# Optimization experiments

Hardware: AMD Instinct MI355X
Metric: run time of the kernel (lower is better)

## Reference

```python
import jax, jax.numpy as jnp
import numpy as np

N_USERS = 60000
N_ITEMS = 40000
N_NODES = N_USERS + N_ITEMS
N_EDGES = 1_000_000
D = 64
BN_EPS = 1e-3  # tf.layers.batch_normalization default epsilon


def setup_inputs() -> dict:
    key = jax.random.key(0)
    ks = jax.random.split(key, 16)
    s = 1.0 / np.sqrt(D)  # uniform-ish init scale for [D,D] weights
    w = lambda k: (jax.random.uniform(k, (D, D), jnp.float32, -1.0, 1.0) * s)
    return {
        "u_features": jax.random.normal(ks[0], (N_USERS, D), jnp.float32),
        "v_features": jax.random.normal(ks[1], (N_ITEMS, D), jnp.float32),
        "edge_start": jax.random.randint(ks[2], (N_EDGES,), 0, N_NODES, jnp.int32),
        "edge_end": jax.random.randint(ks[3], (N_EDGES,), 0, N_NODES, jnp.int32),
        "Ui1": w(ks[4]), "Uj1": w(ks[5]), "Vi1": w(ks[6]), "Vj1": w(ks[7]),
        "bu1": jnp.zeros((D,), jnp.float32), "bv1": jnp.zeros((D,), jnp.float32),
        "Ui2": w(ks[8]), "Uj2": w(ks[9]), "Vi2": w(ks[10]), "Vj2": w(ks[11]),
        "bu2": jnp.zeros((D,), jnp.float32), "bv2": jnp.zeros((D,), jnp.float32),
        "R": w(ks[12]),
        "gamma1": jnp.ones((D,), jnp.float32), "beta1": jnp.zeros((D,), jnp.float32),
        "gamma2": jnp.ones((D,), jnp.float32), "beta2": jnp.zeros((D,), jnp.float32),
    }


def _stage(x, Ui, Uj, Vi, Vj, bu, bv, e_start, e_end, n_nodes):
    # gate = sigmoid(E_end@(x Vi) + E_start@(x Vj) + bv)   -> edge gather
    gate = jax.nn.sigmoid((x @ Vi)[e_end] + (x @ Vj)[e_start] + bv)  # [E, D]
    msg = gate * (x @ Ui)[e_start]                                    # [E, D]
    # x Uj + E_end.T @ msg + bu   -> scatter-add to destination nodes
    agg = jax.ops.segment_sum(msg, e_end, num_segments=n_nodes)       # [N, D]
    return x @ Uj + agg + bu


def _batchnorm(x, gamma, beta):
    mean = jnp.mean(x, axis=0)
    var = jnp.var(x, axis=0)
    return gamma * (x - mean) * jax.lax.rsqrt(var + BN_EPS) + beta


def reference(u_features, v_features, edge_start, edge_end,
              Ui1, Uj1, Vi1, Vj1, bu1, bv1,
              Ui2, Uj2, Vi2, Vj2, bu2, bv2,
              R, gamma1, beta1, gamma2, beta2):
    num_users = u_features.shape[0]
    x_in = jnp.concatenate([u_features, v_features], axis=0)  # [N, D]
    n = x_in.shape[0]
    x = _stage(x_in, Ui1, Uj1, Vi1, Vj1, bu1, bv1, edge_start, edge_end, n)
    x = jax.nn.relu(_batchnorm(x, gamma1, beta1))
    x = _stage(x, Ui2, Uj2, Vi2, Vj2, bu2, bv2, edge_start, edge_end, n)
    x = _batchnorm(x, gamma2, beta2)
    x = jax.nn.relu(x + x_in @ R)  # residual branch
    return x[:num_users], x[num_users:]
```

## Files before the change

### kernel.cpp

```cpp
#include <hip/hip_runtime.h>
#include <hip/hip_bf16.h>

#define NUSERS 60000
#define NNODES 100000
#define DD 64
#define NGB 1563
#define GMM 782
#define NBUK 196
#define ESB 2048

typedef __hip_bfloat16 bf16;
using bf16x8 = __attribute__((ext_vector_type(8))) short;
using f32x4  = __attribute__((ext_vector_type(4))) float;

__device__ __forceinline__ float b2f(bf16 x) { return __bfloat162float(x); }
__device__ __forceinline__ bf16 f2b(float x) { return __float2bfloat16(x); }
__device__ __forceinline__ unsigned short fbits(float x) {
    union { bf16 b; unsigned short u; } cv; cv.b = f2b(x); return cv.u;
}
__device__ __forceinline__ float us2f(unsigned short h) {
    union { unsigned u; float f; } t; t.u = (unsigned)h << 16; return t.f;
}
__device__ __forceinline__ float lo_bf16(unsigned w) {
    union { unsigned u; float f; } t; t.u = w << 16; return t.f;
}
__device__ __forceinline__ float hi_bf16(unsigned w) {
    union { unsigned u; float f; } t; t.u = w & 0xFFFF0000u; return t.f;
}
__device__ __forceinline__ float ldf(const void* p, size_t i, int isbf) {
    if (isbf) return b2f(((const bf16*)p)[i]);
    return ((const float*)p)[i];
}
__device__ __forceinline__ unsigned pack2(float a, float b) {
    return (unsigned)fbits(a) | ((unsigned)fbits(b) << 16);
}
__device__ __forceinline__ unsigned pr2(float x0, float x1, float a0, float a1,
                                        float b0, float b1) {
    float t0 = a0 * x0 + b0, t1 = a1 * x1 + b1;
    t0 = t0 > 0.f ? t0 : 0.f;
    t1 = t1 > 0.f ? t1 : 0.f;
    return pack2(t0, t1);
}

__global__ void k_sniff(const unsigned short* __restrict__ h,
                        int* __restrict__ flag, float* __restrict__ red,
                        int* __restrict__ btot)
{
    __shared__ int cs[256];
    int t = threadIdx.x;
    int cnt = 0;
    for (int i = t; i < 1024; i += 256) {
        int e = (h[2 * i] >> 7) & 0xFF;
        cnt += (e >= 100 && e <= 140) ? 1 : 0;
    }
    cs[t] = cnt;
    __syncthreads();
    for (int s = 128; s > 0; s >>= 1) {
        if (t < s) cs[t] += cs[t + s];
        __syncthreads();
    }
    if (t == 0) flag[0] = (cs[0] > 512) ? 1 : 0;
    red[t] = 0.f;
    btot[t] = 0;
}

__global__ __launch_bounds__(256) void k_bhist(const int* __restrict__ ee,
                                               int* __restrict__ btot, int E)
{
    __shared__ int h[256];
    int t = threadIdx.x;
    h[t] = 0;
    __syncthreads();
    for (int e = blockIdx.x * 256 + t; e < E; e += gridDim.x * 256)
        atomicAdd(&h[ee[e] >> 9], 1);
    __syncthreads();
    if (h[t]) atomicAdd(&btot[t], h[t]);
}

__global__ void k_bscan(const int* __restrict__ btot, int* __restrict__ bbase,
                        int* __restrict__ bcursor)
{
    __shared__ int sd[256];
    int t = threadIdx.x;
    int v = btot[t];
    sd[t] = v;
    __syncthreads();
    for (int off = 1; off < 256; off <<= 1) {
        int x = (t >= off) ? sd[t - off] : 0;
        __syncthreads();
        sd[t] += x;
        __syncthreads();
    }
    int excl = sd[t] - v;
    bbase[t] = excl;
    bcursor[t] = excl;
}

__global__ __launch_bounds__(256) void k_bscatter(
    const int* __restrict__ es, const int* __restrict__ ee,
    int* __restrict__ bcursor, unsigned* __restrict__ ebuf, int E)
{
    __shared__ int h[256], gb[256], lr[256];
    int t = threadIdx.x;
    h[t] = 0;
    lr[t] = 0;
    __syncthreads();
    int base = blockIdx.x * ESB;
    unsigned ent[8];
    int bk[8];
#pragma unroll
    for (int i = 0; i < 8; i++) {
        int e = base + t + i * 256;
        if (e < E) {
            int s = es[e], d = ee[e];
            bk[i] = d >> 9;
            ent[i] = (unsigned)s | ((unsigned)(d & 511) << 20);
            atomicAdd(&h[bk[i]], 1);
        } else bk[i] = -1;
    }
    __syncthreads();
    if (h[t]) gb[t] = atomicAdd(&bcursor[t], h[t]);
    __syncthreads();
#pragma unroll
    for (int i = 0; i < 8; i++) {
        if (bk[i] >= 0) {
            int r = atomicAdd(&lr[bk[i]], 1);
            ebuf[gb[bk[i]] + r] = ent[i];
        }
    }
}

__global__ __launch_bounds__(256) void k_group(
    const int* __restrict__ bbase, const unsigned* __restrict__ ebuf,
    int* __restrict__ rowptr, int* __restrict__ srcidx)
{
    __shared__ int h[512], sc[512];
    int b = blockIdx.x, t = threadIdx.x;
    int lo = bbase[b], hi = bbase[b + 1];
    h[t] = 0;
    h[t + 256] = 0;
    __syncthreads();
    for (int i = lo + t; i < hi; i += 256)
        atomicAdd(&h[ebuf[i] >> 20], 1);
    __syncthreads();
    sc[t] = h[t];
    sc[t + 256] = h[t + 256];
    __syncthreads();
    for (int off = 1; off < 512; off <<= 1) {
        int v0 = (t >= off) ? sc[t - off] : 0;
        int v1 = (t + 256 >= off) ? sc[t + 256 - off] : 0;
        __syncthreads();
        sc[t] += v0;
        sc[t + 256] += v1;
        __syncthreads();
    }
    int n0 = b * 512 + t, n1 = b * 512 + t + 256;
    int e0 = lo + sc[t] - h[t];
    int e1 = lo + sc[t + 256] - h[t + 256];
    if (n0 < NNODES) rowptr[n0] = e0;
    if (n1 < NNODES) rowptr[n1] = e1;
    if (b == NBUK - 1 && t == 0) rowptr[NNODES] = hi;
    h[t] = e0;
    h[t + 256] = e1;
    __syncthreads();
    for (int i = lo + t; i < hi; i += 256) {
        unsigned en = ebuf[i];
        int pos = atomicAdd(&h[en >> 20], 1);
        int s = (int)(en & 0xFFFFF);
        srcidx[pos] = s < NNODES ? s : 0;
    }
}

template <int MODE>
__device__ __forceinline__ void stage_load(
    int tile, int tid, int bfflag,
    const void* u, const void* v, const unsigned short* Aacc,
    const float* ab, uint4& w0, uint4& w1)
{
    int r = tid >> 2, c0 = (tid & 3) * 16;
    int row = tile * DD + r;
    int rowc = row < NNODES ? row : NNODES - 1;
    if (MODE == 0) {
        const void* src = (rowc < NUSERS) ? u : v;
        size_t off = (rowc < NUSERS) ? ((size_t)rowc * DD + c0)
                                     : ((size_t)(rowc - NUSERS) * DD + c0);
        if (bfflag) {
            const uint4* p = (const uint4*)((const unsigned short*)src + off);
            w0 = p[0];
            w1 = p[1];
        } else {
            const float4* p = (const float4*)((const float*)src + off);
            float4 f0 = p[0], f1 = p[1], f2 = p[2], f3 = p[3];
            w0 = make_uint4(pack2(f0.x, f0.y), pack2(f0.z, f0.w),
                            pack2(f1.x, f1.y), pack2(f1.z, f1.w));
            w1 = make_uint4(pack2(f2.x, f2.y), pack2(f2.z, f2.w),
                            pack2(f3.x, f3.y), pack2(f3.z, f3.w));
        }
    } else {
        const uint4* p = (const uint4*)(Aacc + (size_t)rowc * DD + c0);
        unsigned aw[8];
        *(uint4*)&aw[0] = p[0];
        *(uint4*)&aw[4] = p[1];
        const float4* pa = (const float4*)(ab + c0);
        const float4* pb = (const float4*)(ab + 64 + c0);
        float av[16], bv[16];
#pragma unroll
        for (int j = 0; j < 4; j++) {
            float4 fa = pa[j], fb = pb[j];
            av[4 * j] = fa.x; av[4 * j + 1] = fa.y;
            av[4 * j + 2] = fa.z; av[4 * j + 3] = fa.w;
            bv[4 * j] = fb.x; bv[4 * j + 1] = fb.y;
            bv[4 * j + 2] = fb.z; bv[4 * j + 3] = fb.w;
        }
        unsigned ow[8];
#pragma unroll
        for (int j = 0; j < 8; j++)
            ow[j] = pr2(lo_bf16(aw[j]), hi_bf16(aw[j]),
                        av[2 * j], av[2 * j + 1], bv[2 * j], bv[2 * j + 1]);
        w0 = *(uint4*)&ow[0];
        w1 = *(uint4*)&ow[4];
    }
}

__device__ __forceinline__ void stage_store(unsigned short* xbuf, int tid,
                                            const uint4& w0, const uint4& w1)
{
    int r = tid >> 2, c0 = (tid & 3) * 16;
    *(uint4*)&xbuf[r * 72 + c0] = w0;
    *((uint4*)&xbuf[r * 72 + c0] + 1) = w1;
}

template <int MODE>
__global__ __launch_bounds__(256, 4) void k_mm4_mfma(
    const void* __restrict__ u, const void* __restrict__ v,
    const float* __restrict__ red, const void* __restrict__ gm,
    const void* __restrict__ bt,
    const void* __restrict__ W0, const void* __restrict__ W1,
    const void* __restrict__ W2, const void* __restrict__ W3,
    const void* __restrict__ b0, const void* __restrict__ b1,
    const int* __restrict__ flag,
    unsigned short* __restrict__ A, unsigned short* __restrict__ Ed,
    unsigned* __restrict__ Tw)
{
    __shared__ __align__(16) unsigned short lsd[4 * DD * 72];
    __shared__ __align__(16) float abs_s[128];
    const int bfflag = flag[0];
    const int tid = threadIdx.x;

    if (MODE == 1) {
        if (tid < 64) {
            float mean = red[tid] * (1.f / NNODES);
            float var = red[64 + tid] * (1.f / NNODES) - mean * mean;
            float a = ldf(gm, tid, bfflag) * rsqrtf(var + 1e-3f);
            abs_s[tid] = a;
            abs_s[64 + tid] = ldf(bt, tid, bfflag) - mean * a;
        }
        __syncthreads();
    }

    int t = blockIdx.x;
    uint4 xa, xb;
    stage_load<MODE>(t, tid, bfflag, u, v, A, abs_s, xa, xb);

    if (bfflag) {
#define WSTG_BF(m, src)                                                   \
        _Pragma("unroll")                                                 \
        for (int j = 0; j < 2; j++) {                                     \
            int i = tid + j * 256; int e0 = i * 8;                        \
            *(uint4*)&lsd[(m) * 4608 + (e0 >> 6) * 72 + (e0 & 63)] =      \
                ((const uint4*)(src))[i];                                 \
        }
        WSTG_BF(0, W0) WSTG_BF(1, W1) WSTG_BF(2, W2) WSTG_BF(3, W3)
    } else {
#define WSTG_F32(m, src)                                                  \
        _Pragma("unroll")                                                 \
        for (int j = 0; j < 4; j++) {                                     \
            int i = tid + j * 256; int e0 = i * 4;                        \
            float4 f = ((const float4*)(src))[i];                         \
            *(uint2*)&lsd[(m) * 4608 + (e0 >> 6) * 72 + (e0 & 63)] =      \
                make_uint2(pack2(f.x, f.y), pack2(f.z, f.w));             \
        }
        WSTG_F32(0, W0) WSTG_F32(1, W1) WSTG_F32(2, W2) WSTG_F32(3, W3)
    }
    __syncthreads();

    const int wv = tid >> 6, lane = tid & 63;
    const int quad = lane >> 4, ln = lane & 15;
    const int mA = (wv < 2) ? wv : 2;
    bf16x8 bfrA[2][4], bfrB[2][4];
#pragma unroll
    for (int ks = 0; ks < 2; ks++)
#pragma unroll
        for (int nt = 0; nt < 4; nt++)
#pragma unroll
            for (int j = 0; j < 8; j++)
                bfrA[ks][nt][j] = (short)lsd[mA * 4608 +
                    (ks * 32 + quad * 8 + j) * 72 + nt * 16 + ln];
    if (wv >= 2) {
#pragma unroll
        for (int ks = 0; ks < 2; ks++)
#pragma unroll
            for (int nt = 0; nt < 4; nt++)
#pragma unroll
                for (int j = 0; j < 8; j++)
                    bfrB[ks][nt][j] = (short)lsd[3 * 4608 +
                        (ks * 32 + quad * 8 + j) * 72 + nt * 16 + ln];
    }
    float bias[4];
#pragma unroll
    for (int nt = 0; nt < 4; nt++)
        bias[nt] = (wv == 0) ? ldf(b0, nt * 16 + ln, bfflag)
                 : (wv == 1) ? ldf(b1, nt * 16 + ln, bfflag) : 0.f;
    __syncthreads();

    auto compute = [&](const unsigned short* xt, int row0) {
        if (wv < 2) {
#pragma unroll
            for (int rt = 0; rt < 4; rt++) {
                int m = rt * 16 + ln;
                bf16x8 af0 = *(const bf16x8*)&xt[m * 72 + quad * 8];
                bf16x8 af1 = *(const bf16x8*)&xt[m * 72 + 32 + quad * 8];
#pragma unroll
                for (int nt = 0; nt < 4; nt++) {
                    f32x4 c = {0.f, 0.f, 0.f, 0.f};
                    c = __builtin_amdgcn_mfma_f32_16x16x32_bf16(af0, bfrA[0][nt], c, 0, 0, 0);
                    c = __builtin_amdgcn_mfma_f32_16x16x32_bf16(af1, bfrA[1][nt], c, 0, 0, 0);
                    int col = nt * 16 + ln;
#pragma unroll
                    for (int r = 0; r < 4; r++) {
                        int row = row0 + rt * 16 + quad * 4 + r;
                        if (row < NNODES) {
                            size_t o = (size_t)row * DD + col;
                            if (wv == 0) A[o] = fbits(c[r] + bias[nt]);
                            else         Ed[o] = fbits(__expf(-(c[r] + bias[nt])));
                        }
                    }
                }
            }
        } else {
            const int rtb = (wv - 2) * 2;
#pragma unroll
            for (int rr = 0; rr < 2; rr++) {
                int rt = rtb + rr;
                int m = rt * 16 + ln;
                bf16x8 af0 = *(const bf16x8*)&xt[m * 72 + quad * 8];
                bf16x8 af1 = *(const bf16x8*)&xt[m * 72 + 32 + quad * 8];
#pragma unroll
                for (int nt = 0; nt < 4; nt++) {
                    f32x4 c2 = {0.f, 0.f, 0.f, 0.f};
                    f32x4 c3 = {0.f, 0.f, 0.f, 0.f};
                    c2 = __builtin_amdgcn_mfma_f32_16x16x32_bf16(af0, bfrA[0][nt], c2, 0, 0, 0);
                    c2 = __builtin_amdgcn_mfma_f32_16x16x32_bf16(af1, bfrA[1][nt], c2, 0, 0, 0);
                    c3 = __builtin_amdgcn_mfma_f32_16x16x32_bf16(af0, bfrB[0][nt], c3, 0, 0, 0);
                    c3 = __builtin_amdgcn_mfma_f32_16x16x32_bf16(af1, bfrB[1][nt], c3, 0, 0, 0);
                    int col = nt * 16 + ln;
#pragma unroll
                    for (int r = 0; r < 4; r++) {
                        int row = row0 + rt * 16 + quad * 4 + r;
                        if (row < NNODES)
                            Tw[(size_t)row * DD + col] =
                                pack2(c2[r], __expf(-c3[r]));
                    }
                }
            }
        }
    };

    stage_store(lsd, tid, xa, xb);
    int tn = t + GMM;
    if (tn < NGB)
        stage_load<MODE>(tn, tid, bfflag, u, v, A, abs_s, xa, xb);
    __syncthreads();
    int buf = 0;
    while (true) {
        compute(lsd + buf * 4608, t * DD);
        if (tn >= NGB) break;
        t = tn;
        tn += GMM;
        stage_store(lsd + (buf ^ 1) * 4608, tid, xa, xb);
        if (tn < NGB)
            stage_load<MODE>(tn, tid, bfflag, u, v, A, abs_s, xa, xb);
        __syncthreads();
        buf ^= 1;
    }
}

__global__ __launch_bounds__(256) void k_final_mfma(
    const unsigned short* __restrict__ A, const float* __restrict__ red,
    const void* __restrict__ gm, const void* __restrict__ bt,
    const void* __restrict__ u, const void* __restrict__ v,
    const void* __restrict__ R, const int* __restrict__ flag,
    void* __restrict__ out)
{
    __shared__ __align__(16) unsigned short Wls[DD][72];
    __shared__ __align__(16) unsigned short xls[DD][72];
    __shared__ __align__(16) float abf[128];
    const int bfflag = flag[0];
    const int tid = threadIdx.x;
    if (tid < 64) {
        float mean = red[tid] * (1.f / NNODES);
        float var = red[64 + tid] * (1.f / NNODES) - mean * mean;
        float a = ldf(gm, tid, bfflag) * rsqrtf(var + 1e-3f);
        abf[tid] = a;
        abf[64 + tid] = ldf(bt, tid, bfflag) - mean * a;
    }
    if (bfflag) {
        for (int i = tid; i < 512; i += 256) {
            int e0 = i * 8;
            *(uint4*)&Wls[e0 >> 6][e0 & 63] = ((const uint4*)R)[i];
        }
    } else {
        for (int i = tid; i < 1024; i += 256) {
            int e0 = i * 4;
            float4 f = ((const float4*)R)[i];
            *(uint2*)&Wls[e0 >> 6][e0 & 63] =
                make_uint2(pack2(f.x, f.y), pack2(f.z, f.w));
        }
    }
    uint4 w0, w1;
    stage_load<0>(blockIdx.x, tid, bfflag, u, v, nullptr, nullptr, w0, w1);
    stage_store(&xls[0][0], tid, w0, w1);
    __syncthreads();

    const int row0 = blockIdx.x * DD;
    const int wv = tid >> 6, lane = tid & 63;
    const int quad = lane >> 4, ln = lane & 15;
    bf16x8 bfr[2][4];
#pragma unroll
    for (int ks = 0; ks < 2; ks++)
#pragma unroll
        for (int nt = 0; nt < 4; nt++)
#pragma unroll
            for (int j = 0; j < 8; j++)
                bfr[ks][nt][j] = (short)Wls[ks * 32 + quad * 8 + j][nt * 16 + ln];
    float av[4], bv[4];
#pragma unroll
    for (int nt = 0; nt < 4; nt++) {
        av[nt] = abf[nt * 16 + ln];
        bv[nt] = abf[64 + nt * 16 + ln];
    }
    const int rt = wv;
    int m = rt * 16 + ln;
    bf16x8 af0 = *(const bf16x8*)&xls[m][quad * 8];
    bf16x8 af1 = *(const bf16x8*)&xls[m][32 + quad * 8];
#pragma unroll
    for (int nt = 0; nt < 4; nt++) {
        f32x4 c = {0.f, 0.f, 0.f, 0.f};
        c = __builtin_amdgcn_mfma_f32_16x16x32_bf16(af0, bfr[0][nt], c, 0, 0, 0);
        c = __builtin_amdgcn_mfma_f32_16x16x32_bf16(af1, bfr[1][nt], c, 0, 0, 0);
        int col = nt * 16 + ln;
#pragma unroll
        for (int r = 0; r < 4; r++) {
            int row = row0 + rt * 16 + quad * 4 + r;
            if (row < NNODES) {
                size_t o = (size_t)row * DD + col;
                float vv = av[nt] * us2f(A[o]) + bv[nt] + c[r];
                vv = vv > 0.f ? vv : 0.f;
                if (bfflag) ((unsigned short*)out)[o] = fbits(vv);
                else        ((float*)out)[o] = vv;
            }
        }
    }
}

__global__ __launch_bounds__(256) void k_accum(
    const int* __restrict__ rowptr, const int* __restrict__ srcidx,
    const unsigned* __restrict__ T, const bf16* __restrict__ Ed,
    unsigned short* __restrict__ A)
{
    int d = blockIdx.x * 4 + (threadIdx.x >> 6);
    if (d >= NNODES) return;
    int c = threadIdx.x & 63;
    int r0 = rowptr[d], r1 = rowptr[d + 1];
    size_t o = (size_t)d * DD + c;
    float ed = b2f(Ed[o]);
    float sum = us2f(A[o]);
    int i = r0;
#define EDGE(tv) sum += lo_bf16(tv) * \
    __builtin_amdgcn_rcpf(1.f + ed * hi_bf16(tv));
    for (; i + 7 < r1; i += 8) {
        unsigned t0 = T[(size_t)srcidx[i] * DD + c];
        unsigned t1 = T[(size_t)srcidx[i + 1] * DD + c];
        unsigned t2 = T[(size_t)srcidx[i + 2] * DD + c];
        unsigned t3 = T[(size_t)srcidx[i + 3] * DD + c];
        unsigned t4 = T[(size_t)srcidx[i + 4] * DD + c];
        unsigned t5 = T[(size_t)srcidx[i + 5] * DD + c];
        unsigned t6 = T[(size_t)srcidx[i + 6] * DD + c];
        unsigned t7 = T[(size_t)srcidx[i + 7] * DD + c];
        EDGE(t0) EDGE(t1) EDGE(t2) EDGE(t3)
        EDGE(t4) EDGE(t5) EDGE(t6) EDGE(t7)
    }
    for (; i + 3 < r1; i += 4) {
        unsigned t0 = T[(size_t)srcidx[i] * DD + c];
        unsigned t1 = T[(size_t)srcidx[i + 1] * DD + c];
        unsigned t2 = T[(size_t)srcidx[i + 2] * DD + c];
        unsigned t3 = T[(size_t)srcidx[i + 3] * DD + c];
        EDGE(t0) EDGE(t1) EDGE(t2) EDGE(t3)
    }
    for (; i < r1; i++) {
        unsigned t = T[(size_t)srcidx[i] * DD + c];
        EDGE(t)
    }
#undef EDGE
    A[o] = fbits(sum);
}

__global__ __launch_bounds__(256) void k_reduce(
    const unsigned short* __restrict__ x, float* __restrict__ red)
{
    __shared__ float s1[256], s2[256];
    const int c = threadIdx.x & 63, rg = threadIdx.x >> 6;
    float sum = 0.f, sq = 0.f;
    for (int row = blockIdx.x * 4 + rg; row < NNODES; row += gridDim.x * 4) {
        float vv = us2f(x[(size_t)row * DD + c]);
        sum += vv;
        sq += vv * vv;
    }
    s1[threadIdx.x] = sum;
    s2[threadIdx.x] = sq;
    __syncthreads();
    if (threadIdx.x < 64) {
        sum = s1[c] + s1[64 + c] + s1[128 + c] + s1[192 + c];
        sq = s2[c] + s2[64 + c] + s2[128 + c] + s2[192 + c];
        unsafeAtomicAdd(&red[c], sum);
        unsafeAtomicAdd(&red[64 + c], sq);
    }
}

extern "C" void kernel_launch(void* const* d_in, const int* in_sizes, int n_in,
                              void* d_out, int out_size, void* d_ws, size_t ws_size,
                              hipStream_t stream)
{
    const void* u   = d_in[0];
    const void* v   = d_in[1];
    const int* es   = (const int*)d_in[2];
    const int* ee   = (const int*)d_in[3];
    const void* Ui1 = d_in[4];
    const void* Uj1 = d_in[5];
    const void* Vi1 = d_in[6];
    const void* Vj1 = d_in[7];
    const void* bu1 = d_in[8];
    const void* bv1 = d_in[9];
    const void* Ui2 = d_in[10];
    const void* Uj2 = d_in[11];
    const void* Vi2 = d_in[12];
    const void* Vj2 = d_in[13];
    const void* bu2 = d_in[14];
    const void* bv2 = d_in[15];
    const void* R   = d_in[16];
    const void* g1  = d_in[17];
    const void* be1 = d_in[18];
    const void* g2  = d_in[19];
    const void* be2 = d_in[20];
    const int E = in_sizes[2];

    char* ws = (char*)d_ws;
    unsigned short* A = (unsigned short*)(ws);
    unsigned* T    = (unsigned*)(ws + 25600000);
    unsigned* ebuf = (unsigned*)(ws + 25600000);
    int* srcidx    = (int*)(ws + 51200000);
    int* rowptr    = (int*)(ws + 56000000);
    float* red     = (float*)(ws + 56802176);
    int* flag      = (int*)(ws + 56804224);
    int* btot      = (int*)(ws + 56804352);
    int* bbase     = (int*)(ws + 56805376);
    int* bcursor   = (int*)(ws + 56806400);
    float* red1 = red, *red2 = red + 128;
    bf16* Ed = (bf16*)d_out;

    k_sniff<<<1, 256, 0, stream>>>((const unsigned short*)u, flag, red, btot);
    k_bhist<<<400, 256, 0, stream>>>(ee, btot, E);
    k_bscan<<<1, 256, 0, stream>>>(btot, bbase, bcursor);
    k_bscatter<<<(E + ESB - 1) / ESB, 256, 0, stream>>>(es, ee, bcursor, ebuf, E);
    k_group<<<NBUK, 256, 0, stream>>>(bbase, ebuf, rowptr, srcidx);

    k_mm4_mfma<0><<<GMM, 256, 0, stream>>>(u, v, nullptr, nullptr, nullptr,
                                           Uj1, Vi1, Ui1, Vj1, bu1, bv1, flag,
                                           A, (unsigned short*)Ed, T);
    k_accum<<<(NNODES + 3) / 4, 256, 0, stream>>>(rowptr, srcidx, T, Ed, A);
    k_reduce<<<1024, 256, 0, stream>>>(A, red1);

    k_mm4_mfma<1><<<GMM, 256, 0, stream>>>(nullptr, nullptr, red1, g1, be1,
                                           Uj2, Vi2, Ui2, Vj2, bu2, bv2, flag,
                                           A, (unsigned short*)Ed, T);
    k_accum<<<(NNODES + 3) / 4, 256, 0, stream>>>(rowptr, srcidx, T, Ed, A);
    k_reduce<<<1024, 256, 0, stream>>>(A, red2);

    k_final_mfma<<<NGB, 256, 0, stream>>>(A, red2, g2, be2, u, v, R, flag, d_out);
}
```

Before: 392.6 us.

## Merge sniff into histogram, shard BN reductions, and process two nodes per wave

Folds the dtype sniff kernel into the histogram kernel. Per-block histograms are now written out non-atomically and summed in the scan kernel, which also zeroes the reduction buffers. The batch-norm statistics reduction is unrolled four rows per thread and spreads its atomics across 8 shards to cut atomic contention, with consumers summing the shards. The accumulate kernel handles two destination nodes per wave to amortise block overhead. In exchange, the scan kernel serially reads 400 partial histograms, and the reused workspace regions must not overlap live data.

```diff
diff --git a/kernel.cpp b/kernel.cpp
--- a/kernel.cpp
+++ b/kernel.cpp
@@ -8,6 +8,7 @@
 #define GMM 782
 #define NBUK 196
 #define ESB 2048
+#define NBH 400
 
 typedef __hip_bfloat16 bf16;
 using bf16x8 = __attribute__((ext_vector_type(8))) short;
@@ -42,47 +43,42 @@
     return pack2(t0, t1);
 }
 
-__global__ void k_sniff(const unsigned short* __restrict__ h,
-                        int* __restrict__ flag, float* __restrict__ red,
-                        int* __restrict__ btot)
-{
-    __shared__ int cs[256];
-    int t = threadIdx.x;
-    int cnt = 0;
-    for (int i = t; i < 1024; i += 256) {
-        int e = (h[2 * i] >> 7) & 0xFF;
-        cnt += (e >= 100 && e <= 140) ? 1 : 0;
-    }
-    cs[t] = cnt;
-    __syncthreads();
-    for (int s = 128; s > 0; s >>= 1) {
-        if (t < s) cs[t] += cs[t + s];
-        __syncthreads();
-    }
-    if (t == 0) flag[0] = (cs[0] > 512) ? 1 : 0;
-    red[t] = 0.f;
-    btot[t] = 0;
-}
-
-__global__ __launch_bounds__(256) void k_bhist(const int* __restrict__ ee,
-                                               int* __restrict__ btot, int E)
+__global__ __launch_bounds__(256) void k_bhist(
+    const int* __restrict__ ee, const unsigned short* __restrict__ hsn,
+    int* __restrict__ flag, int* __restrict__ bh, int E)
 {
     __shared__ int h[256];
     int t = threadIdx.x;
+    if (blockIdx.x == 0) {
+        int cnt = 0;
+        for (int i = t; i < 1024; i += 256) {
+            int e = (hsn[2 * i] >> 7) & 0xFF;
+            cnt += (e >= 100 && e <= 140) ? 1 : 0;
+        }
+        h[t] = cnt;
+        __syncthreads();
+        for (int s = 128; s > 0; s >>= 1) {
+            if (t < s) h[t] += h[t + s];
+            __syncthreads();
+        }
+        if (t == 0) flag[0] = (h[0] > 512) ? 1 : 0;
+        __syncthreads();
+    }
     h[t] = 0;
     __syncthreads();
     for (int e = blockIdx.x * 256 + t; e < E; e += gridDim.x * 256)
         atomicAdd(&h[ee[e] >> 9], 1);
     __syncthreads();
-    if (h[t]) atomicAdd(&btot[t], h[t]);
-}
-
-__global__ void k_bscan(const int* __restrict__ btot, int* __restrict__ bbase,
-                        int* __restrict__ bcursor)
+    bh[blockIdx.x * 256 + t] = h[t];
+}
+
+__global__ void k_bscan(const int* __restrict__ bh, int* __restrict__ bbase,
+                        int* __restrict__ bcursor, float* __restrict__ redz)
 {
     __shared__ int sd[256];
     int t = threadIdx.x;
-    int v = btot[t];
+    int v = 0;
+    for (int b = 0; b < NBH; b++) v += bh[b * 256 + t];
     sd[t] = v;
     __syncthreads();
     for (int off = 1; off < 256; off <<= 1) {
@@ -94,6 +90,7 @@
     int excl = sd[t] - v;
     bbase[t] = excl;
     bcursor[t] = excl;
+    for (int i = t; i < 4096; i += 256) redz[i] = 0.f;
 }
 
 __global__ __launch_bounds__(256) void k_bscatter(
@@ -249,8 +246,14 @@
 
     if (MODE == 1) {
         if (tid < 64) {
-            float mean = red[tid] * (1.f / NNODES);
-            float var = red[64 + tid] * (1.f / NNODES) - mean * mean;
+            float sm = 0.f, sq = 0.f;
+#pragma unroll
+            for (int s = 0; s < 8; s++) {
+                sm += red[s * 256 + tid];
+                sq += red[s * 256 + 128 + tid];
+            }
+            float mean = sm * (1.f / NNODES);
+            float var = sq * (1.f / NNODES) - mean * mean;
             float a = ldf(gm, tid, bfflag) * rsqrtf(var + 1e-3f);
             abs_s[tid] = a;
             abs_s[64 + tid] = ldf(bt, tid, bfflag) - mean * a;
@@ -398,8 +401,14 @@
     const int bfflag = flag[0];
     const int tid = threadIdx.x;
     if (tid < 64) {
-        float mean = red[tid] * (1.f / NNODES);
-        float var = red[64 + tid] * (1.f / NNODES) - mean * mean;
+        float sm = 0.f, sq = 0.f;
+#pragma unroll
+        for (int s = 0; s < 8; s++) {
+            sm += red[s * 256 + tid];
+            sq += red[s * 256 + 128 + tid];
+        }
+        float mean = sm * (1.f / NNODES);
+        float var = sq * (1.f / NNODES) - mean * mean;
         float a = ldf(gm, tid, bfflag) * rsqrtf(var + 1e-3f);
         abf[tid] = a;
         abf[64 + tid] = ldf(bt, tid, bfflag) - mean * a;
@@ -468,41 +477,54 @@
     const unsigned* __restrict__ T, const bf16* __restrict__ Ed,
     unsigned short* __restrict__ A)
 {
-    int d = blockIdx.x * 4 + (threadIdx.x >> 6);
-    if (d >= NNODES) return;
-    int c = threadIdx.x & 63;
-    int r0 = rowptr[d], r1 = rowptr[d + 1];
-    size_t o = (size_t)d * DD + c;
-    float ed = b2f(Ed[o]);
-    float sum = us2f(A[o]);
-    int i = r0;
-#define EDGE(tv) sum += lo_bf16(tv) * \
-    __builtin_amdgcn_rcpf(1.f + ed * hi_bf16(tv));
-    for (; i + 7 < r1; i += 8) {
-        unsigned t0 = T[(size_t)srcidx[i] * DD + c];
-        unsigned t1 = T[(size_t)srcidx[i + 1] * DD + c];
-        unsigned t2 = T[(size_t)srcidx[i + 2] * DD + c];
-        unsigned t3 = T[(size_t)srcidx[i + 3] * DD + c];
-        unsigned t4 = T[(size_t)srcidx[i + 4] * DD + c];
-        unsigned t5 = T[(size_t)srcidx[i + 5] * DD + c];
-        unsigned t6 = T[(size_t)srcidx[i + 6] * DD + c];
-        unsigned t7 = T[(size_t)srcidx[i + 7] * DD + c];
-        EDGE(t0) EDGE(t1) EDGE(t2) EDGE(t3)
-        EDGE(t4) EDGE(t5) EDGE(t6) EDGE(t7)
-    }
-    for (; i + 3 < r1; i += 4) {
-        unsigned t0 = T[(size_t)srcidx[i] * DD + c];
-        unsigned t1 = T[(size_t)srcidx[i + 1] * DD + c];
-        unsigned t2 = T[(size_t)srcidx[i + 2] * DD + c];
-        unsigned t3 = T[(size_t)srcidx[i + 3] * DD + c];
-        EDGE(t0) EDGE(t1) EDGE(t2) EDGE(t3)
-    }
-    for (; i < r1; i++) {
-        unsigned t = T[(size_t)srcidx[i] * DD + c];
-        EDGE(t)
-    }
+    const int wv = threadIdx.x >> 6, c = threadIdx.x & 63;
+    int d1 = blockIdx.x * 8 + wv;
+    int d2 = d1 + 4;
+    int p0 = rowptr[d1], p1 = rowptr[d1 + 1];
+    int q0 = rowptr[d2], q1 = rowptr[d2 + 1];
+    size_t o1 = (size_t)d1 * DD + c, o2 = (size_t)d2 * DD + c;
+    float ed1 = b2f(Ed[o1]), ed2 = b2f(Ed[o2]);
+    float sum1 = us2f(A[o1]), sum2 = us2f(A[o2]);
+
+#define EDGE(sv, edv, tv) sv += lo_bf16(tv) * \
+    __builtin_amdgcn_rcpf(1.f + edv * hi_bf16(tv));
+#define NODE_LOOP(sv, edv, r0, r1)                                  \
+    {                                                               \
+        int i = r0;                                                 \
+        for (; i + 7 < r1; i += 8) {                                \
+            unsigned t0 = T[(size_t)srcidx[i] * DD + c];            \
+            unsigned t1 = T[(size_t)srcidx[i + 1] * DD + c];        \
+            unsigned t2 = T[(size_t)srcidx[i + 2] * DD + c];        \
+            unsigned t3 = T[(size_t)srcidx[i + 3] * DD + c];        \
+            unsigned t4 = T[(size_t)srcidx[i + 4] * DD + c];        \
+            unsigned t5 = T[(size_t)srcidx[i + 5] * DD + c];        \
+            unsigned t6 = T[(size_t)srcidx[i + 6] * DD + c];        \
+            unsigned t7 = T[(size_t)srcidx[i + 7] * DD + c];        \
+            EDGE(sv, edv, t0) EDGE(sv, edv, t1)                     \
+            EDGE(sv, edv, t2) EDGE(sv, edv, t3)                     \
+            EDGE(sv, edv, t4) EDGE(sv, edv, t5)                     \
+            EDGE(sv, edv, t6) EDGE(sv, edv, t7)                     \
+        }                                                           \
+        for (; i + 3 < r1; i += 4) {                                \
+            unsigned t0 = T[(size_t)srcidx[i] * DD + c];            \
+            unsigned t1 = T[(size_t)srcidx[i + 1] * DD + c];        \
+            unsigned t2 = T[(size_t)srcidx[i + 2] * DD + c];        \
+            unsigned t3 = T[(size_t)srcidx[i + 3] * DD + c];        \
+            EDGE(sv, edv, t0) EDGE(sv, edv, t1)                     \
+            EDGE(sv, edv, t2) EDGE(sv, edv, t3)                     \
+        }                                                           \
+        for (; i < r1; i++) {                                       \
+            unsigned t0 = T[(size_t)srcidx[i] * DD + c];            \
+            EDGE(sv, edv, t0)                                       \
+        }                                                           \
+    }
+
+    NODE_LOOP(sum1, ed1, p0, p1)
+    A[o1] = fbits(sum1);
+    NODE_LOOP(sum2, ed2, q0, q1)
+    A[o2] = fbits(sum2);
+#undef NODE_LOOP
 #undef EDGE
-    A[o] = fbits(sum);
 }
 
 __global__ __launch_bounds__(256) void k_reduce(
@@ -510,20 +532,28 @@
 {
     __shared__ float s1[256], s2[256];
     const int c = threadIdx.x & 63, rg = threadIdx.x >> 6;
-    float sum = 0.f, sq = 0.f;
-    for (int row = blockIdx.x * 4 + rg; row < NNODES; row += gridDim.x * 4) {
-        float vv = us2f(x[(size_t)row * DD + c]);
-        sum += vv;
-        sq += vv * vv;
-    }
-    s1[threadIdx.x] = sum;
-    s2[threadIdx.x] = sq;
+    float a0 = 0.f, a1 = 0.f, a2 = 0.f, a3 = 0.f;
+    float q0 = 0.f, q1 = 0.f, q2 = 0.f, q3 = 0.f;
+    for (int row = blockIdx.x * 16 + rg * 4; row < NNODES;
+         row += gridDim.x * 16) {
+        float v0 = us2f(x[(size_t)row * DD + c]);
+        float v1 = (row + 1 < NNODES) ? us2f(x[(size_t)(row + 1) * DD + c]) : 0.f;
+        float v2 = (row + 2 < NNODES) ? us2f(x[(size_t)(row + 2) * DD + c]) : 0.f;
+        float v3 = (row + 3 < NNODES) ? us2f(x[(size_t)(row + 3) * DD + c]) : 0.f;
+        a0 += v0; q0 += v0 * v0;
+        a1 += v1; q1 += v1 * v1;
+        a2 += v2; q2 += v2 * v2;
+        a3 += v3; q3 += v3 * v3;
+    }
+    s1[threadIdx.x] = (a0 + a1) + (a2 + a3);
+    s2[threadIdx.x] = (q0 + q1) + (q2 + q3);
     __syncthreads();
     if (threadIdx.x < 64) {
-        sum = s1[c] + s1[64 + c] + s1[128 + c] + s1[192 + c];
-        sq = s2[c] + s2[64 + c] + s2[128 + c] + s2[192 + c];
-        unsafeAtomicAdd(&red[c], sum);
-        unsafeAtomicAdd(&red[64 + c], sq);
+        float sum = s1[c] + s1[64 + c] + s1[128 + c] + s1[192 + c];
+        float sq = s2[c] + s2[64 + c] + s2[128 + c] + s2[192 + c];
+        float* sh = red + (blockIdx.x & 7) * 256;
+        unsafeAtomicAdd(&sh[c], sum);
+        unsafeAtomicAdd(&sh[128 + c], sq);
     }
 }
 
@@ -559,31 +589,31 @@
     unsigned* T    = (unsigned*)(ws + 25600000);
     unsigned* ebuf = (unsigned*)(ws + 25600000);
     int* srcidx    = (int*)(ws + 51200000);
+    int* bh        = (int*)(ws + 51200000);
+    float* redsh   = (float*)(ws + 55200000);
     int* rowptr    = (int*)(ws + 56000000);
-    float* red     = (float*)(ws + 56802176);
     int* flag      = (int*)(ws + 56804224);
-    int* btot      = (int*)(ws + 56804352);
     int* bbase     = (int*)(ws + 56805376);
     int* bcursor   = (int*)(ws + 56806400);
-    float* red1 = red, *red2 = red + 128;
+    float* red1 = redsh;
+    float* red2 = redsh + 2048;
     bf16* Ed = (bf16*)d_out;
 
-    k_sniff<<<1, 256, 0, stream>>>((const unsigned short*)u, flag, red, btot);
-    k_bhist<<<400, 256, 0, stream>>>(ee, btot, E);
-    k_bscan<<<1, 256, 0, stream>>>(btot, bbase, bcursor);
+    k_bhist<<<NBH, 256, 0, stream>>>(ee, (const unsigned short*)u, flag, bh, E);
+    k_bscan<<<1, 256, 0, stream>>>(bh, bbase, bcursor, redsh);
     k_bscatter<<<(E + ESB - 1) / ESB, 256, 0, stream>>>(es, ee, bcursor, ebuf, E);
     k_group<<<NBUK, 256, 0, stream>>>(bbase, ebuf, rowptr, srcidx);
 
     k_mm4_mfma<0><<<GMM, 256, 0, stream>>>(u, v, nullptr, nullptr, nullptr,
                                            Uj1, Vi1, Ui1, Vj1, bu1, bv1, flag,
                                            A, (unsigned short*)Ed, T);
-    k_accum<<<(NNODES + 3) / 4, 256, 0, stream>>>(rowptr, srcidx, T, Ed, A);
+    k_accum<<<NNODES / 8, 256, 0, stream>>>(rowptr, srcidx, T, Ed, A);
     k_reduce<<<1024, 256, 0, stream>>>(A, red1);
 
     k_mm4_mfma<1><<<GMM, 256, 0, stream>>>(nullptr, nullptr, red1, g1, be1,
                                            Uj2, Vi2, Ui2, Vj2, bu2, bv2, flag,
                                            A, (unsigned short*)Ed, T);
-    k_accum<<<(NNODES + 3) / 4, 256, 0, stream>>>(rowptr, srcidx, T, Ed, A);
+    k_accum<<<NNODES / 8, 256, 0, stream>>>(rowptr, srcidx, T, Ed, A);
     k_reduce<<<1024, 256, 0, stream>>>(A, red2);
 
     k_final_mfma<<<NGB, 256, 0, stream>>>(A, red2, g2, be2, u, v, R, flag, d_out);
```

Measured after the change: 345.0 us. -12.1%, faster.
